# Optimization experiments

Measured on AMD Instinct MI355X. Metric: run time of the kernel, lower is better.

## Reference

```python
import jax, jax.numpy as jnp
import numpy as np
from jax import lax

EPS_DIST = 1e-6   # matches 1/(distances + 1e-6)
EPS_SQRT = 1e-12  # guard sqrt at zero


def setup_inputs() -> dict:
    key = jax.random.key(0)
    kq, ks = jax.random.split(key)
    query = jax.random.normal(kq, (2048, 32, 16), dtype=jnp.float32)
    support = jax.random.normal(ks, (65536, 32, 16), dtype=jnp.float32)
    return {"query": query, "support": support, "k": 16}


def reference(query, support, k):
    # Flatten (N, D, H) -> (N, D*H)
    q = query.reshape(query.shape[0], -1)   # (N_q, F)
    s = support.reshape(support.shape[0], -1)  # (N_s, F)
    # Euclidean distances via ||q||^2 + ||s||^2 - 2 q s^T
    q2 = jnp.sum(q * q, axis=1, keepdims=True)          # (N_q, 1)
    s2 = jnp.sum(s * s, axis=1)                          # (N_s,)
    d2 = q2 + s2[None, :] - 2.0 * (q @ s.T)              # (N_q, N_s)
    dist = jnp.sqrt(jnp.maximum(d2, EPS_SQRT))           # (N_q, N_s)
    # k smallest distances (sorted ascending, like sklearn kneighbors)
    neg_topk, indices = lax.top_k(-dist, k)              # (N_q, k)
    dist_k = -neg_topk
    sim = 1.0 / (dist_k + EPS_DIST)
    weights = sim / jnp.sum(sim, axis=1, keepdims=True)
    return indices, weights.astype(jnp.float32)
```

## Files before the change

### kernel.cpp

```cpp
#include <hip/hip_runtime.h>
#include <math.h>
#include <stdint.h>

#define NQ   2048
#define NS   65536
#define FDIM 512
#define KSEL 16
#define LDA  132
#define LDB  320
#define LDT  132

typedef _Float16 f16x8 __attribute__((ext_vector_type(8)));
typedef float    f32x16 __attribute__((ext_vector_type(16)));

#define GLL16(dst, src)                                                        \
  __builtin_amdgcn_global_load_lds(                                            \
      (const __attribute__((address_space(1))) void*)(src),                    \
      (__attribute__((address_space(3))) void*)(dst), 16, 0, 0)

#define BAR_NOVM() asm volatile("s_waitcnt lgkmcnt(0)\ns_barrier" ::: "memory")

#define MFMA16(a, b, c) __builtin_amdgcn_mfma_f32_32x32x16_f16((a), (b), (c), 0, 0, 0)

__global__ void knn_norms(const float* __restrict__ q, const float* __restrict__ s,
                          float* __restrict__ q2, float* __restrict__ s2) {
  int wid  = (int)blockIdx.x * 4 + ((int)threadIdx.x >> 6);
  int lane = threadIdx.x & 63;
  if (wid >= NQ + NS) return;
  const float* src = (wid < NQ) ? (q + (size_t)wid * FDIM)
                                : (s + (size_t)(wid - NQ) * FDIM);
  float acc = 0.f;
#pragma unroll
  for (int j = 0; j < FDIM / 256; ++j) {
    float4 v = *(const float4*)&src[(lane + 64 * j) * 4];
    acc = fmaf(v.x, v.x, acc); acc = fmaf(v.y, v.y, acc);
    acc = fmaf(v.z, v.z, acc); acc = fmaf(v.w, v.w, acc);
  }
#pragma unroll
  for (int off = 32; off; off >>= 1) acc += __shfl_xor(acc, off, 64);
  if (lane == 0) {
    if (wid < NQ) q2[wid] = acc;
    else          s2[wid - NQ] = acc;
  }
}

__global__ void knn_prep(const float* __restrict__ q, const float* __restrict__ s,
                         float* __restrict__ q2, float* __restrict__ s2,
                         _Float16* __restrict__ qh, _Float16* __restrict__ ql,
                         _Float16* __restrict__ sh, _Float16* __restrict__ slo) {
  const int wgl = (int)blockIdx.x * 4 + ((int)threadIdx.x >> 6);
  const int ln  = threadIdx.x & 63;
  const int lm  = ln & 31;
  const int lh  = ln >> 5;
  constexpr int NRBQ = NQ / 32;
  constexpr int NRB  = (NQ + NS) / 32;
  if (wgl >= NRB) return;
  const bool isq = wgl < NRBQ;
  const int rb = isq ? wgl : wgl - NRBQ;
  const float* src = (isq ? q : s) + ((size_t)rb * 32 + lm) * FDIM + lh * 8;
  _Float16* hp = (isq ? qh : sh)  + (size_t)rb * (32 * FDIM);
  _Float16* lp = (isq ? ql : slo) + (size_t)rb * (32 * FDIM);
  const float scale = isq ? -2.f : 1.f;
  float acc = 0.f;
#pragma unroll 4
  for (int kb = 0; kb < FDIM / 16; ++kb) {
    float4 v0 = *(const float4*)&src[kb * 16];
    float4 v1 = *(const float4*)&src[kb * 16 + 4];
    const float x[8] = {v0.x, v0.y, v0.z, v0.w, v1.x, v1.y, v1.z, v1.w};
    f16x8 hv, lv;
#pragma unroll
    for (int j = 0; j < 8; ++j) {
      acc = fmaf(x[j], x[j], acc);
      float xs = x[j] * scale;
      _Float16 h = (_Float16)xs;
      hv[j] = h;
      lv[j] = (_Float16)(xs - (float)h);
    }
    *(f16x8*)&hp[(size_t)kb * 512 + ln * 8] = hv;
    *(f16x8*)&lp[(size_t)kb * 512 + ln * 8] = lv;
  }
  acc += __shfl_xor(acc, 32, 64);
  if (ln < 32) {
    if (isq) q2[rb * 32 + lm] = acc;
    else     s2[rb * 32 + lm] = acc;
  }
}

template <int CT>
__device__ __forceinline__ void sel_slice2(
    const f32x16 (&acc)[4][2], float (&ld)[KSEL], int (&li)[KSEL],
    float (*scr)[257], const float* s2c,
    int wv, int lm, int lh, int srow, int shalf, int s0, int slp) {
  BAR_NOVM();
  if ((wv & 3) == slp) {
    const int c = lm;
    const float s2v = s2c[slp * 64 + CT * 32 + c];
    const int rb = (wv >> 2) * 128;
#pragma unroll
    for (int rt = 0; rt < 4; ++rt)
#pragma unroll
      for (int r = 0; r < 16; ++r) {
        const int row = rb + rt * 32 + (r & 3) + 8 * (r >> 2) + 4 * lh;
        scr[c][row] = acc[rt][CT][r] + s2v;
      }
  }
  BAR_NOVM();
  const int cbase = s0 + slp * 64 + CT * 32 + shalf * 16;
  for (int c = 0; c < 16; ++c) {
    const float ev = scr[shalf * 16 + c][srow];
    if (ev < ld[KSEL - 1]) {
      bool lt[KSEL];
#pragma unroll
      for (int s = 0; s < KSEL; ++s) lt[s] = ev < ld[s];
      const int iv = cbase + c;
#pragma unroll
      for (int s = KSEL - 1; s >= 1; --s) {
        ld[s] = lt[s - 1] ? ld[s - 1] : (lt[s] ? ev : ld[s]);
        li[s] = lt[s - 1] ? li[s - 1] : (lt[s] ? iv : li[s]);
      }
      if (lt[0]) { ld[0] = ev; li[0] = iv; }
    }
  }
}

template <int NCHUNK>
__global__ __launch_bounds__(512, 2) void knn_phase1_mfma256(
    const _Float16* __restrict__ qh, const _Float16* __restrict__ ql,
    const _Float16* __restrict__ sh, const _Float16* __restrict__ sl_,
    const float* __restrict__ s2g,
    float* __restrict__ cand_e, int* __restrict__ cand_i) {
  constexpr int CHUNKSZ = NS / NCHUNK;
  constexpr int NST     = CHUNKSZ / 256;
  constexpr int NT      = NST * 32;
  constexpr int BUFH    = 16384;

  __shared__ __align__(16) _Float16 stg[3 * BUFH];
  __shared__ __align__(16) float scr[32][257];
  __shared__ __align__(16) float s2all[CHUNKSZ];

  const int tid = threadIdx.x;
  const int wv  = tid >> 6;
  const int ln  = tid & 63;
  const int lm  = ln & 31;
  const int lh  = ln >> 5;
  const int wr  = wv >> 2;
  const int wc  = wv & 3;
  const int q0  = (int)blockIdx.x * 256;
  const int chunk = blockIdx.y;
  const int rbA  = q0 >> 5;
  const int rbB0 = chunk * (CHUNKSZ >> 5);

  float ld[KSEL]; int li[KSEL];
#pragma unroll
  for (int s = 0; s < KSEL; ++s) { ld[s] = INFINITY; li[s] = 0x7fffffff; }
  const int srow  = tid >> 1;
  const int shalf = tid & 1;
  const size_t lo = (size_t)ln * 8;

  {
    float4 v = *(const float4*)&s2g[(size_t)chunk * CHUNKSZ + tid * 4];
    *(float4*)&s2all[tid * 4] = v;
    asm volatile("s_waitcnt lgkmcnt(0)" ::: "memory");
  }

  auto STAGE = [&](int b, int t) {
    const int st_ = t >> 5, kb_ = t & 31;
    _Float16* d = stg + b * BUFH;
    const size_t ak = ((size_t)(rbA + wv) * 32 + kb_) * 512 + lo;
    const size_t bk = ((size_t)(rbB0 + st_ * 8 + wv) * 32 + kb_) * 512 + lo;
    GLL16(d +         wv * 512, qh  + ak);
    GLL16(d +  4096 + wv * 512, ql  + ak);
    GLL16(d +  8192 + wv * 512, sh  + bk);
    GLL16(d + 12288 + wv * 512, sl_ + bk);
  };

  STAGE(0, 0);
  STAGE(1, 1);
  asm volatile("s_waitcnt vmcnt(4)" ::: "memory");
  __builtin_amdgcn_s_barrier();
  int b0 = 0, b1 = 1, b2 = 2;

#pragma unroll 1
  for (int st = 0; st < NST; ++st) {
    const int s0 = chunk * CHUNKSZ + st * 256;

    f32x16 acc[4][2];
#pragma unroll
    for (int rt = 0; rt < 4; ++rt)
#pragma unroll
      for (int ct = 0; ct < 2; ++ct)
#pragma unroll
        for (int r = 0; r < 16; ++r) acc[rt][ct][r] = 0.f;

#pragma unroll 1
    for (int kb = 0; kb < 32; ++kb) {
      const int t = st * 32 + kb;
      const _Float16* base = stg + b0 * BUFH;

      f16x8 bh0 = *(const f16x8*)&base[ 8192 + (wc * 2 + 0) * 512 + ln * 8];
      f16x8 bh1 = *(const f16x8*)&base[ 8192 + (wc * 2 + 1) * 512 + ln * 8];
      f16x8 bl0 = *(const f16x8*)&base[12288 + (wc * 2 + 0) * 512 + ln * 8];
      f16x8 bl1 = *(const f16x8*)&base[12288 + (wc * 2 + 1) * 512 + ln * 8];
      f16x8 a0h = *(const f16x8*)&base[       (wr * 4 + 0) * 512 + ln * 8];
      f16x8 a0l = *(const f16x8*)&base[4096 + (wr * 4 + 0) * 512 + ln * 8];
      f16x8 a1h = *(const f16x8*)&base[       (wr * 4 + 1) * 512 + ln * 8];
      f16x8 a1l = *(const f16x8*)&base[4096 + (wr * 4 + 1) * 512 + ln * 8];
      if (t + 2 < NT) STAGE(b2, t + 2);
      __builtin_amdgcn_s_barrier();
      asm volatile("s_waitcnt lgkmcnt(0)" ::: "memory");
      __builtin_amdgcn_sched_barrier(0);
      __builtin_amdgcn_s_setprio(1);
      acc[0][0] = MFMA16(a0h, bh0, acc[0][0]);
      acc[0][1] = MFMA16(a0h, bh1, acc[0][1]);
      acc[0][0] = MFMA16(a0h, bl0, acc[0][0]);
      acc[0][1] = MFMA16(a0h, bl1, acc[0][1]);
      acc[0][0] = MFMA16(a0l, bh0, acc[0][0]);
      acc[0][1] = MFMA16(a0l, bh1, acc[0][1]);
      acc[1][0] = MFMA16(a1h, bh0, acc[1][0]);
      acc[1][1] = MFMA16(a1h, bh1, acc[1][1]);
      acc[1][0] = MFMA16(a1h, bl0, acc[1][0]);
      acc[1][1] = MFMA16(a1h, bl1, acc[1][1]);
      acc[1][0] = MFMA16(a1l, bh0, acc[1][0]);
      acc[1][1] = MFMA16(a1l, bh1, acc[1][1]);
      __builtin_amdgcn_s_setprio(0);
      __builtin_amdgcn_s_barrier();

      f16x8 a2h = *(const f16x8*)&base[       (wr * 4 + 2) * 512 + ln * 8];
      f16x8 a2l = *(const f16x8*)&base[4096 + (wr * 4 + 2) * 512 + ln * 8];
      f16x8 a3h = *(const f16x8*)&base[       (wr * 4 + 3) * 512 + ln * 8];
      f16x8 a3l = *(const f16x8*)&base[4096 + (wr * 4 + 3) * 512 + ln * 8];
      if (t < NT - 2)      { asm volatile("s_waitcnt vmcnt(4)" ::: "memory"); }
      else if (t == NT - 2){ asm volatile("s_waitcnt vmcnt(0)" ::: "memory"); }
      __builtin_amdgcn_s_barrier();
      asm volatile("s_waitcnt lgkmcnt(0)" ::: "memory");
      __builtin_amdgcn_sched_barrier(0);
      __builtin_amdgcn_s_setprio(1);
      acc[2][0] = MFMA16(a2h, bh0, acc[2][0]);
      acc[2][1] = MFMA16(a2h, bh1, acc[2][1]);
      acc[2][0] = MFMA16(a2h, bl0, acc[2][0]);
      acc[2][1] = MFMA16(a2h, bl1, acc[2][1]);
      acc[2][0] = MFMA16(a2l, bh0, acc[2][0]);
      acc[2][1] = MFMA16(a2l, bh1, acc[2][1]);
      acc[3][0] = MFMA16(a3h, bh0, acc[3][0]);
      acc[3][1] = MFMA16(a3h, bh1, acc[3][1]);
      acc[3][0] = MFMA16(a3h, bl0, acc[3][0]);
      acc[3][1] = MFMA16(a3h, bl1, acc[3][1]);
      acc[3][0] = MFMA16(a3l, bh0, acc[3][0]);
      acc[3][1] = MFMA16(a3l, bh1, acc[3][1]);
      __builtin_amdgcn_s_setprio(0);
      __builtin_amdgcn_s_barrier();

      const int tmp = b0; b0 = b1; b1 = b2; b2 = tmp;
    }

#pragma unroll 1
    for (int slp = 0; slp < 4; ++slp) {
      sel_slice2<0>(acc, ld, li, scr, s2all + st * 256, wv, lm, lh, srow, shalf, s0, slp);
      sel_slice2<1>(acc, ld, li, scr, s2all + st * 256, wv, lm, lh, srow, shalf, s0, slp);
    }
  }

  const size_t base =
      ((size_t)(q0 + srow) * NCHUNK + chunk) * (2 * KSEL) + shalf * KSEL;
#pragma unroll
  for (int j = 0; j < KSEL; ++j) {
    cand_e[base + j] = ld[j];
    cand_i[base + j] = li[j];
  }
}

template <int NCHUNK, int HALVES>
__global__ __launch_bounds__(256, 2) void knn_phase1(
    const float* __restrict__ query, const float* __restrict__ support,
    const float* __restrict__ s2g,
    float* __restrict__ cand_e, int* __restrict__ cand_i) {
  constexpr int CHUNKSZ = NS / NCHUNK;
  constexpr int NST = CHUNKSZ / 256;

  __shared__ __align__(16) float AsT[16][LDA];
  __shared__ __align__(16) float BsT[16 * LDB];
  __shared__ __align__(16) float scrT[64][LDT];
  __shared__ float s2s[256];

  const int tid = threadIdx.x;
  const int tx  = tid & 15;
  const int ty  = tid >> 4;
  const int q0  = (int)blockIdx.x * 128;
  const int chunk = blockIdx.y;

  float ld[KSEL]; int li[KSEL];
#pragma unroll
  for (int s = 0; s < KSEL; ++s) { ld[s] = INFINITY; li[s] = 0x7fffffff; }
  const int  srow  = (HALVES == 2) ? (tid >> 1) : tid;
  const int  shalf = (HALVES == 2) ? (tid & 1) : 0;
  const bool scan_active = (HALVES == 2) || (tid < 128);

  for (int st = 0; st < NST; ++st) {
    const int s0 = chunk * CHUNKSZ + st * 256;
    s2s[tid] = s2g[s0 + tid];

    float acc[8][16];
#pragma unroll
    for (int i = 0; i < 8; ++i)
#pragma unroll
      for (int j = 0; j < 16; ++j) acc[i][j] = 0.f;

    float4 pa[2], pb[4];
    const int rr = tid >> 2, cq = tid & 3, cc = cq << 2;

#pragma unroll
    for (int p = 0; p < 2; ++p)
      pa[p] = *(const float4*)&query[(size_t)(q0 + rr + 64 * p) * FDIM + cc];
#pragma unroll
    for (int p = 0; p < 4; ++p)
      pb[p] = *(const float4*)&support[(size_t)(s0 + rr + 64 * p) * FDIM + cc];

    for (int kb = 0; kb < FDIM / 16; ++kb) {
      __syncthreads();
#pragma unroll
      for (int p = 0; p < 2; ++p) {
        const int r = rr + 64 * p;
        const float v[4] = {pa[p].x, pa[p].y, pa[p].z, pa[p].w};
#pragma unroll
        for (int j = 0; j < 4; ++j) AsT[cq * 4 + j][r] = v[j];
      }
#pragma unroll
      for (int p = 0; p < 4; ++p) {
        const int r  = rr + 64 * p;
        const int pc = 20 * (r >> 4) + (r & 15);
        const float v[4] = {pb[p].x, pb[p].y, pb[p].z, pb[p].w};
#pragma unroll
        for (int j = 0; j < 4; ++j) BsT[(cq * 4 + j) * LDB + pc] = v[j];
      }
      if (kb + 1 < FDIM / 16) {
        const int kc = (kb + 1) * 16 + cc;
#pragma unroll
        for (int p = 0; p < 2; ++p)
          pa[p] = *(const float4*)&query[(size_t)(q0 + rr + 64 * p) * FDIM + kc];
#pragma unroll
        for (int p = 0; p < 4; ++p)
          pb[p] = *(const float4*)&support[(size_t)(s0 + rr + 64 * p) * FDIM + kc];
      }
      __syncthreads();
#pragma unroll 4
      for (int kk = 0; kk < 16; ++kk) {
        float4 a0 = *(const float4*)&AsT[kk][ty * 8];
        float4 a1 = *(const float4*)&AsT[kk][ty * 8 + 4];
        const float* brow = &BsT[kk * LDB + 20 * tx];
        float4 b0 = *(const float4*)&brow[0];
        float4 b1 = *(const float4*)&brow[4];
        float4 b2 = *(const float4*)&brow[8];
        float4 b3 = *(const float4*)&brow[12];
        const float a[8]  = {a0.x, a0.y, a0.z, a0.w, a1.x, a1.y, a1.z, a1.w};
        const float b[16] = {b0.x, b0.y, b0.z, b0.w, b1.x, b1.y, b1.z, b1.w,
                             b2.x, b2.y, b2.z, b2.w, b3.x, b3.y, b3.z, b3.w};
#pragma unroll
        for (int i = 0; i < 8; ++i)
#pragma unroll
          for (int j = 0; j < 16; ++j)
            acc[i][j] = fmaf(a[i], b[j], acc[i][j]);
      }
    }

#pragma unroll 1
    for (int sl = 0; sl < 4; ++sl) {
      __syncthreads();
      if ((tx >> 2) == sl) {
        const int csb = (tx & 3) * 16;
#pragma unroll
        for (int j = 0; j < 16; ++j) {
          const float s2v = s2s[tx * 16 + j];
          float4 v0, v1;
          v0.x = fmaf(-2.f, acc[0][j], s2v);
          v0.y = fmaf(-2.f, acc[1][j], s2v);
          v0.z = fmaf(-2.f, acc[2][j], s2v);
          v0.w = fmaf(-2.f, acc[3][j], s2v);
          v1.x = fmaf(-2.f, acc[4][j], s2v);
          v1.y = fmaf(-2.f, acc[5][j], s2v);
          v1.z = fmaf(-2.f, acc[6][j], s2v);
          v1.w = fmaf(-2.f, acc[7][j], s2v);
          *(float4*)&scrT[csb + j][ty * 8]     = v0;
          *(float4*)&scrT[csb + j][ty * 8 + 4] = v1;
        }
      }
      __syncthreads();
      if (scan_active) {
        const int cbase = s0 + sl * 64 + shalf * 32;
        const int ccount = (HALVES == 2) ? 32 : 64;
        const int coff   = (HALVES == 2) ? shalf * 32 : 0;
        for (int c = 0; c < ccount; ++c) {
          const float ev = scrT[coff + c][srow];
          if (ev < ld[KSEL - 1]) {
            bool lt[KSEL];
#pragma unroll
            for (int s = 0; s < KSEL; ++s) lt[s] = ev < ld[s];
            const int iv = cbase + c;
#pragma unroll
            for (int s = KSEL - 1; s >= 1; --s) {
              ld[s] = lt[s - 1] ? ld[s - 1] : (lt[s] ? ev : ld[s]);
              li[s] = lt[s - 1] ? li[s - 1] : (lt[s] ? iv : li[s]);
            }
            if (lt[0]) { ld[0] = ev; li[0] = iv; }
          }
        }
      }
    }
  }

  if (scan_active) {
    const size_t base =
        ((size_t)(q0 + srow) * NCHUNK + chunk) * (HALVES * KSEL) + shalf * KSEL;
#pragma unroll
    for (int j = 0; j < KSEL; ++j) {
      cand_e[base + j] = ld[j];
      cand_i[base + j] = li[j];
    }
  }
}

template <int NCAND>
__global__ __launch_bounds__(64) void knn_phase2(
    const float* __restrict__ cand_e, const int* __restrict__ cand_i,
    const float* __restrict__ q2g, float* __restrict__ out) {
  constexpr int SLOTS = NCAND / 64;
  __shared__ float wd[KSEL];
  __shared__ int   wi[KSEL];

  const int q    = blockIdx.x;
  const int lane = threadIdx.x;
  const float q2 = q2g[q];
  const float* ce = cand_e + (size_t)q * NCAND;
  const int*   ci = cand_i + (size_t)q * NCAND;

  float d[SLOTS]; int idx[SLOTS];
#pragma unroll
  for (int s = 0; s < SLOTS; ++s) {
    d[s]   = q2 + ce[lane + 64 * s];
    idx[s] = ci[lane + 64 * s];
  }

  for (int r = 0; r < KSEL; ++r) {
    float bd = INFINITY; int bi = 0x7fffffff;
#pragma unroll
    for (int s = 0; s < SLOTS; ++s) {
      bool better = (d[s] < bd) || (d[s] == bd && idx[s] < bi);
      if (better) { bd = d[s]; bi = idx[s]; }
    }
#pragma unroll
    for (int off = 32; off; off >>= 1) {
      float od = __shfl_xor(bd, off, 64);
      int   oi = __shfl_xor(bi, off, 64);
      if (od < bd || (od == bd && oi < bi)) { bd = od; bi = oi; }
    }
#pragma unroll
    for (int s = 0; s < SLOTS; ++s)
      if (idx[s] == bi) { d[s] = INFINITY; idx[s] = 0x7fffffff; }
    if (lane == 0) { wd[r] = bd; wi[r] = bi; }
  }
  __syncthreads();

  float sim = 0.f;
  if (lane < KSEL) {
    const float dist = sqrtf(fmaxf(wd[lane], 1e-12f));
    sim = 1.f / (dist + 1e-6f);
  }
  float tot = sim;
#pragma unroll
  for (int off = 8; off; off >>= 1) tot += __shfl_xor(tot, off, 64);
  if (lane < KSEL) {
    out[(size_t)q * KSEL + lane] = (float)wi[lane];
    out[(size_t)NQ * KSEL + (size_t)q * KSEL + lane] = sim / tot;
  }
}

extern "C" void kernel_launch(void* const* d_in, const int* in_sizes, int n_in,
                              void* d_out, int out_size, void* d_ws, size_t ws_size,
                              hipStream_t stream) {
  const float* query   = (const float*)d_in[0];
  const float* support = (const float*)d_in[1];
  float* out = (float*)d_out;

  float* q2     = (float*)d_ws;
  float* s2     = q2 + NQ;
  float* cand_e = s2 + NS;

  constexpr int NCHUNK = 32;
  const size_t cand_elems = (size_t)NQ * NCHUNK * 2 * KSEL;
  const size_t plane_off  = (size_t)(NQ + NS) + 2 * cand_elems;
  const size_t half_elems = 2 * (size_t)(NQ + NS) * FDIM;
  const size_t need_mfma  = plane_off * 4 + half_elems * 2;
  const size_t need2 = (size_t)(NQ + NS + 2 * NQ * NCHUNK * 2 * KSEL) * 4;

  if (ws_size >= need_mfma) {
    int* cand_i = (int*)(cand_e + cand_elems);
    _Float16* qh  = (_Float16*)((float*)d_ws + plane_off);
    _Float16* ql  = qh + (size_t)NQ * FDIM;
    _Float16* shp = ql + (size_t)NQ * FDIM;
    _Float16* slp = shp + (size_t)NS * FDIM;
    knn_prep<<<(NQ + NS) / (32 * 4), 256, 0, stream>>>(query, support, q2, s2,
                                                       qh, ql, shp, slp);
    dim3 g1(NQ / 256, NCHUNK);
    knn_phase1_mfma256<NCHUNK><<<g1, 512, 0, stream>>>(qh, ql, shp, slp, s2,
                                                       cand_e, cand_i);
    knn_phase2<NCHUNK * 2 * KSEL><<<NQ, 64, 0, stream>>>(cand_e, cand_i, q2, out);
  } else {
    knn_norms<<<(NQ + NS) / 4, 256, 0, stream>>>(query, support, q2, s2);
    if (ws_size >= need2) {
      int* cand_i = (int*)(cand_e + (size_t)NQ * NCHUNK * 2 * KSEL);
      dim3 g1(NQ / 128, NCHUNK);
      knn_phase1<NCHUNK, 2><<<g1, 256, 0, stream>>>(query, support, s2, cand_e, cand_i);
      knn_phase2<NCHUNK * 2 * KSEL><<<NQ, 64, 0, stream>>>(cand_e, cand_i, q2, out);
    } else {
      int* cand_i = (int*)(cand_e + (size_t)NQ * NCHUNK * KSEL);
      dim3 g1(NQ / 128, NCHUNK);
      knn_phase1<NCHUNK, 1><<<g1, 256, 0, stream>>>(query, support, s2, cand_e, cand_i);
      knn_phase2<NCHUNK * KSEL><<<NQ, 64, 0, stream>>>(cand_e, cand_i, q2, out);
    }
  }
}
```

Baseline: 867.6 us.

## Swap GEMM operand roles so selection runs in registers without LDS transpose

```diff
diff --git a/kernel.cpp b/kernel.cpp
--- a/kernel.cpp
+++ b/kernel.cpp
@@ -17,8 +17,6 @@
   __builtin_amdgcn_global_load_lds(                                            \
       (const __attribute__((address_space(1))) void*)(src),                    \
       (__attribute__((address_space(3))) void*)(dst), 16, 0, 0)
-
-#define BAR_NOVM() asm volatile("s_waitcnt lgkmcnt(0)\ns_barrier" ::: "memory")
 
 #define MFMA16(a, b, c) __builtin_amdgcn_mfma_f32_32x32x16_f16((a), (b), (c), 0, 0, 0)
 
@@ -86,40 +84,57 @@
   }
 }
 
-template <int CT>
-__device__ __forceinline__ void sel_slice2(
-    const f32x16 (&acc)[4][2], float (&ld)[KSEL], int (&li)[KSEL],
-    float (*scr)[257], const float* s2c,
-    int wv, int lm, int lh, int srow, int shalf, int s0, int slp) {
-  BAR_NOVM();
-  if ((wv & 3) == slp) {
-    const int c = lm;
-    const float s2v = s2c[slp * 64 + CT * 32 + c];
-    const int rb = (wv >> 2) * 128;
-#pragma unroll
-    for (int rt = 0; rt < 4; ++rt)
-#pragma unroll
-      for (int r = 0; r < 16; ++r) {
-        const int row = rb + rt * 32 + (r & 3) + 8 * (r >> 2) + 4 * lh;
-        scr[c][row] = acc[rt][CT][r] + s2v;
-      }
-  }
-  BAR_NOVM();
-  const int cbase = s0 + slp * 64 + CT * 32 + shalf * 16;
-  for (int c = 0; c < 16; ++c) {
-    const float ev = scr[shalf * 16 + c][srow];
-    if (ev < ld[KSEL - 1]) {
-      bool lt[KSEL];
-#pragma unroll
-      for (int s = 0; s < KSEL; ++s) lt[s] = ev < ld[s];
-      const int iv = cbase + c;
-#pragma unroll
-      for (int s = KSEL - 1; s >= 1; --s) {
-        ld[s] = lt[s - 1] ? ld[s - 1] : (lt[s] ? ev : ld[s]);
-        li[s] = lt[s - 1] ? li[s - 1] : (lt[s] ? iv : li[s]);
-      }
-      if (lt[0]) { ld[0] = ev; li[0] = iv; }
-    }
+__device__ __forceinline__ void ins16(float ev, int iv,
+                                      float (&ld)[KSEL], int (&li)[KSEL]) {
+  if (ev < ld[KSEL - 1]) {
+    bool lt[KSEL];
+#pragma unroll
+    for (int s = 0; s < KSEL; ++s) lt[s] = ev < ld[s];
+#pragma unroll
+    for (int s = KSEL - 1; s >= 1; --s) {
+      ld[s] = lt[s - 1] ? ld[s - 1] : (lt[s] ? ev : ld[s]);
+      li[s] = lt[s - 1] ? li[s - 1] : (lt[s] ? iv : li[s]);
+    }
+    if (lt[0]) { ld[0] = ev; li[0] = iv; }
+  }
+}
+
+__device__ __forceinline__ void merge_write(float (&LD)[KSEL], int (&LI)[KSEL],
+                                            int lh, int qq, int chunk, int wr,
+                                            int nchunk,
+                                            float* __restrict__ ce,
+                                            int* __restrict__ ci) {
+  float pv[KSEL]; int pi[KSEL];
+#pragma unroll
+  for (int j = 0; j < KSEL; ++j) {
+    pv[j] = __shfl_xor(LD[j], 32, 64);
+    pi[j] = __shfl_xor(LI[j], 32, 64);
+  }
+  float mv[KSEL]; int mi[KSEL];
+#pragma unroll
+  for (int k = 0; k < KSEL; ++k) {
+    float a = LD[k], b = pv[KSEL - 1 - k];
+    int  ai = LI[k], bi = pi[KSEL - 1 - k];
+    bool t = (a < b) || (a == b && ai < bi);
+    mv[k] = t ? a : b; mi[k] = t ? ai : bi;
+  }
+#pragma unroll
+  for (int d = 8; d >= 1; d >>= 1) {
+#pragma unroll
+    for (int k = 0; k < KSEL; ++k) {
+      if ((k & d) == 0) {
+        float x = mv[k], y = mv[k | d];
+        int  xi = mi[k], yi = mi[k | d];
+        bool sw = (y < x) || (y == x && yi < xi);
+        mv[k] = sw ? y : x;     mi[k] = sw ? yi : xi;
+        mv[k | d] = sw ? x : y; mi[k | d] = sw ? xi : yi;
+      }
+    }
+  }
+  if (lh == 0) {
+    const size_t cb = ((size_t)qq * nchunk + chunk) * (2 * KSEL) + wr * KSEL;
+#pragma unroll
+    for (int j = 0; j < KSEL; ++j) { ce[cb + j] = mv[j]; ci[cb + j] = mi[j]; }
   }
 }
 
@@ -135,7 +150,6 @@
   constexpr int BUFH    = 16384;
 
   __shared__ __align__(16) _Float16 stg[3 * BUFH];
-  __shared__ __align__(16) float scr[32][257];
   __shared__ __align__(16) float s2all[CHUNKSZ];
 
   const int tid = threadIdx.x;
@@ -150,11 +164,12 @@
   const int rbA  = q0 >> 5;
   const int rbB0 = chunk * (CHUNKSZ >> 5);
 
-  float ld[KSEL]; int li[KSEL];
-#pragma unroll
-  for (int s = 0; s < KSEL; ++s) { ld[s] = INFINITY; li[s] = 0x7fffffff; }
-  const int srow  = tid >> 1;
-  const int shalf = tid & 1;
+  float ld0[KSEL], ld1[KSEL]; int li0[KSEL], li1[KSEL];
+#pragma unroll
+  for (int s = 0; s < KSEL; ++s) {
+    ld0[s] = INFINITY; li0[s] = 0x7fffffff;
+    ld1[s] = INFINITY; li1[s] = 0x7fffffff;
+  }
   const size_t lo = (size_t)ln * 8;
 
   {
@@ -166,12 +181,12 @@
   auto STAGE = [&](int b, int t) {
     const int st_ = t >> 5, kb_ = t & 31;
     _Float16* d = stg + b * BUFH;
-    const size_t ak = ((size_t)(rbA + wv) * 32 + kb_) * 512 + lo;
-    const size_t bk = ((size_t)(rbB0 + st_ * 8 + wv) * 32 + kb_) * 512 + lo;
-    GLL16(d +         wv * 512, qh  + ak);
-    GLL16(d +  4096 + wv * 512, ql  + ak);
-    GLL16(d +  8192 + wv * 512, sh  + bk);
-    GLL16(d + 12288 + wv * 512, sl_ + bk);
+    const size_t sk = ((size_t)(rbB0 + st_ * 8 + wv) * 32 + kb_) * 512 + lo;
+    const size_t qk = ((size_t)(rbA + wv) * 32 + kb_) * 512 + lo;
+    GLL16(d +         wv * 512, sh  + sk);
+    GLL16(d +  4096 + wv * 512, sl_ + sk);
+    GLL16(d +  8192 + wv * 512, qh  + qk);
+    GLL16(d + 12288 + wv * 512, ql  + qk);
   };
 
   STAGE(0, 0);
@@ -182,8 +197,6 @@
 
 #pragma unroll 1
   for (int st = 0; st < NST; ++st) {
-    const int s0 = chunk * CHUNKSZ + st * 256;
-
     f32x16 acc[4][2];
 #pragma unroll
     for (int rt = 0; rt < 4; ++rt)
@@ -253,20 +266,24 @@
       const int tmp = b0; b0 = b1; b1 = b2; b2 = tmp;
     }
 
-#pragma unroll 1
-    for (int slp = 0; slp < 4; ++slp) {
-      sel_slice2<0>(acc, ld, li, scr, s2all + st * 256, wv, lm, lh, srow, shalf, s0, slp);
-      sel_slice2<1>(acc, ld, li, scr, s2all + st * 256, wv, lm, lh, srow, shalf, s0, slp);
-    }
-  }
-
-  const size_t base =
-      ((size_t)(q0 + srow) * NCHUNK + chunk) * (2 * KSEL) + shalf * KSEL;
-#pragma unroll
-  for (int j = 0; j < KSEL; ++j) {
-    cand_e[base + j] = ld[j];
-    cand_i[base + j] = li[j];
-  }
+    const int sbase = chunk * CHUNKSZ + st * 256;
+#pragma unroll
+    for (int rt = 0; rt < 4; ++rt) {
+#pragma unroll
+      for (int r = 0; r < 16; ++r) {
+        const int row = wr * 128 + rt * 32 + (r & 3) + 8 * (r >> 2) + 4 * lh;
+        const float s2v = s2all[st * 256 + row];
+        const int iv = sbase + row;
+        ins16(acc[rt][0][r] + s2v, iv, ld0, li0);
+        ins16(acc[rt][1][r] + s2v, iv, ld1, li1);
+      }
+    }
+  }
+
+  merge_write(ld0, li0, lh, q0 + wc * 64 + 0 * 32 + lm, chunk, wr, NCHUNK,
+              cand_e, cand_i);
+  merge_write(ld1, li1, lh, q0 + wc * 64 + 1 * 32 + lm, chunk, wr, NCHUNK,
+              cand_e, cand_i);
 }
 
 template <int NCHUNK, int HALVES>
```

Result: slower. 1.249 ms (+44.0%).
